# Optimization experiments

Hardware: AMD Instinct MI355X
Metric: run time of the kernel (lower is better)

## Reference

```python
import jax, jax.numpy as jnp
import numpy as np

B, T, D, H = 2, 2048, 1024, 16
DH = D // H
TOPK = 64


def setup_inputs() -> dict:
    key = jax.random.key(0)
    ks = jax.random.split(key, 10)
    s = D ** -0.5
    x = jax.random.normal(ks[0], (B, T, D), dtype=jnp.float32)
    key_padding_mask = jax.random.bernoulli(ks[1], 0.1, (B, T))
    Wq = jax.random.normal(ks[2], (D, D), dtype=jnp.float32) * s
    bq = jnp.zeros((D,), dtype=jnp.float32)
    Wk = jax.random.normal(ks[3], (D, D), dtype=jnp.float32) * s
    bk = jnp.zeros((D,), dtype=jnp.float32)
    Wv = jax.random.normal(ks[4], (D, D), dtype=jnp.float32) * s
    bv = jnp.zeros((D,), dtype=jnp.float32)
    Wo = jax.random.normal(ks[5], (D, D), dtype=jnp.float32) * s
    bo = jnp.zeros((D,), dtype=jnp.float32)
    return {"x": x, "Wq": Wq, "bq": bq, "Wk": Wk, "bk": bk,
            "Wv": Wv, "bv": bv, "Wo": Wo, "bo": bo,
            "key_padding_mask": key_padding_mask, "causal": 1}


def _attention(x, Wq, bq, Wk, bk, Wv, bv, Wo, bo, key_padding_mask, causal):
    b, t, d = x.shape
    dh = d // H

    def heads(y):  # (B,T,D) -> (B,H,T,Dh)
        return y.reshape(b, t, H, dh).transpose(0, 2, 1, 3)

    q = heads(x @ Wq.T + bq)
    k = heads(x @ Wk.T + bk)
    v = heads(x @ Wv.T + bv)

    scale = dh ** -0.5
    logits = jnp.einsum('bhqd,bhkd->bhqk', q, k) * scale  # (B,H,T,T)
    neg = jnp.finfo(logits.dtype).min

    # key padding mask: True blocks key position
    logits = jnp.where(key_padding_mask[:, None, None, :], neg, logits)

    if causal:
        i = jnp.arange(t)[:, None]
        j = jnp.arange(t)[None, :]
        blocked = j > (t - t + i)  # Tq == Tk
        logits = jnp.where(blocked[None, None], neg, logits)

    # hard top-k sparsification: keep top-k logits per row, rest -> -inf
    flat = logits.reshape(-1, t)  # (B*H*T, T)
    vals, idx = jax.lax.top_k(flat, TOPK)
    rows = jnp.arange(flat.shape[0])[:, None]
    sparse = jnp.full_like(flat, neg).at[rows, idx].set(vals)
    sparse = sparse.reshape(logits.shape)

    attn = jax.nn.softmax(sparse, axis=-1)
    out = jnp.einsum('bhqk,bhkd->bhqd', attn, v)  # (B,H,T,Dh)
    out = out.transpose(0, 2, 1, 3).reshape(b, t, d)
    return out @ Wo.T + bo


def reference(x, Wq, bq, Wk, bk, Wv, bv, Wo, bo, key_padding_mask, causal):
    return _attention(x, Wq, bq, Wk, bk, Wv, bv, Wo, bo, key_padding_mask, causal)
```

## Files before the change

kernel.cpp:

```cpp
#include <hip/hip_runtime.h>
#include <hip/hip_bf16.h>
#include <stdint.h>

#define BB 2
#define TT 2048
#define DD 1024
#define NH 16
#define HD 64
#define TOPK 64
#define NEGF (-3.402823466e38f)
#define ORD_NEG 0x00800000u
#define QT 16
#define KT 256
#define SELCAP 96

typedef short short8x __attribute__((ext_vector_type(8)));
typedef float floatx4 __attribute__((ext_vector_type(4)));

__device__ __forceinline__ uint32_t ord_u32(float x) {
    uint32_t b = __float_as_uint(x);
    return (b & 0x80000000u) ? ~b : (b | 0x80000000u);
}
__device__ __forceinline__ float unord(uint32_t u) {
    uint32_t b = (u & 0x80000000u) ? (u ^ 0x80000000u) : ~u;
    return __uint_as_float(b);
}
__device__ __forceinline__ short bf16_rne(float x) {
    uint32_t u = __float_as_uint(x);
    u += 0x7FFFu + ((u >> 16) & 1u);
    return (short)(u >> 16);
}
__device__ __forceinline__ float bf16_to_f(short h) {
    return __uint_as_float(((uint32_t)(uint16_t)h) << 16);
}
__device__ __forceinline__ bool mask_at(const void* m, int mode, int idx) {
    if (mode == 0) return ((const int*)m)[idx] != 0;
    if (mode == 1) return ((const unsigned char*)m)[idx] != 0;
    return ((const float*)m)[idx] != 0.0f;
}

__device__ __forceinline__ int dpp_wsum(int v) {
    v += __builtin_amdgcn_update_dpp(0, v, 0x111, 0xf, 0xf, true);
    v += __builtin_amdgcn_update_dpp(0, v, 0x112, 0xf, 0xf, true);
    v += __builtin_amdgcn_update_dpp(0, v, 0x114, 0xf, 0xf, true);
    v += __builtin_amdgcn_update_dpp(0, v, 0x118, 0xf, 0xf, true);
    v += __builtin_amdgcn_update_dpp(0, v, 0x142, 0xa, 0xf, true);
    v += __builtin_amdgcn_update_dpp(0, v, 0x143, 0xc, 0xf, true);
    return __builtin_amdgcn_readlane(v, 63);
}
__device__ __forceinline__ uint32_t dpp_wumax(uint32_t v) {
    uint32_t t;
    t = (uint32_t)__builtin_amdgcn_update_dpp(0, (int)v, 0x111, 0xf, 0xf, true); v = v > t ? v : t;
    t = (uint32_t)__builtin_amdgcn_update_dpp(0, (int)v, 0x112, 0xf, 0xf, true); v = v > t ? v : t;
    t = (uint32_t)__builtin_amdgcn_update_dpp(0, (int)v, 0x114, 0xf, 0xf, true); v = v > t ? v : t;
    t = (uint32_t)__builtin_amdgcn_update_dpp(0, (int)v, 0x118, 0xf, 0xf, true); v = v > t ? v : t;
    t = (uint32_t)__builtin_amdgcn_update_dpp(0, (int)v, 0x142, 0xa, 0xf, true); v = v > t ? v : t;
    t = (uint32_t)__builtin_amdgcn_update_dpp(0, (int)v, 0x143, 0xc, 0xf, true); v = v > t ? v : t;
    return (uint32_t)__builtin_amdgcn_readlane((int)v, 63);
}
__device__ __forceinline__ float dpp_fsum(float v) {
    v += __uint_as_float((uint32_t)__builtin_amdgcn_update_dpp(0, (int)__float_as_uint(v), 0x111, 0xf, 0xf, true));
    v += __uint_as_float((uint32_t)__builtin_amdgcn_update_dpp(0, (int)__float_as_uint(v), 0x112, 0xf, 0xf, true));
    v += __uint_as_float((uint32_t)__builtin_amdgcn_update_dpp(0, (int)__float_as_uint(v), 0x114, 0xf, 0xf, true));
    v += __uint_as_float((uint32_t)__builtin_amdgcn_update_dpp(0, (int)__float_as_uint(v), 0x118, 0xf, 0xf, true));
    v += __uint_as_float((uint32_t)__builtin_amdgcn_update_dpp(0, (int)__float_as_uint(v), 0x142, 0xa, 0xf, true));
    v += __uint_as_float((uint32_t)__builtin_amdgcn_update_dpp(0, (int)__float_as_uint(v), 0x143, 0xc, 0xf, true));
    return __uint_as_float((uint32_t)__builtin_amdgcn_readlane((int)__float_as_uint(v), 63));
}

__global__ void __launch_bounds__(1024) build_flags(
    const unsigned char* raw, const int* causalp, int* flags, uint32_t* Mt)
{
    __shared__ int odd_nz, big, s_mode;
    __shared__ uint32_t smt[BB * 64];
    const int tid = threadIdx.x;
    if (tid == 0) { odd_nz = 0; big = 0; }
    if (tid < BB * 64) smt[tid] = 0;
    __syncthreads();
    for (int i = tid; i < BB * TT; i += 1024) {
        unsigned char c = raw[i];
        if ((i & 3) && c) atomicOr(&odd_nz, 1);
        if (c > 1) atomicOr(&big, 1);
    }
    __syncthreads();
    if (tid == 0) {
        int mode = odd_nz ? (big ? 2 : 1) : 0;
        s_mode = mode;
        flags[0] = mode;
        flags[1] = (causalp[0] != 0) ? 1 : 0;
    }
    __syncthreads();
    const int mode = s_mode;
    const int w = tid >> 3, g = tid & 7;
    const int bb = w >> 6, l = w & 63;
    uint32_t bits = 0;
#pragma unroll
    for (int si = 0; si < 4; ++si) {
        int s = g * 4 + si;
        if (mask_at(raw, mode, bb * TT + l + 64 * s)) bits |= (1u << s);
    }
    if (bits) atomicOr(&smt[w], bits);
    __syncthreads();
    if (tid < BB * 64) Mt[tid] = smt[tid];
}

__global__ void __launch_bounds__(256) split_f32(
    const float* __restrict__ in, short* __restrict__ hi, short* __restrict__ lo,
    int n4, float scale)
{
    int i = blockIdx.x * blockDim.x + threadIdx.x;
    if (i >= n4) return;
    float4 v = ((const float4*)in)[i];
    float f[4] = {v.x * scale, v.y * scale, v.z * scale, v.w * scale};
    short hh[4], ll[4];
#pragma unroll
    for (int j = 0; j < 4; ++j) {
        hh[j] = bf16_rne(f[j]);
        ll[j] = bf16_rne(f[j] - bf16_to_f(hh[j]));
    }
    short4 h4; h4.x = hh[0]; h4.y = hh[1]; h4.z = hh[2]; h4.w = hh[3];
    short4 l4; l4.x = ll[0]; l4.y = ll[1]; l4.z = ll[2]; l4.w = ll[3];
    ((short4*)hi)[i] = h4;
    ((short4*)lo)[i] = l4;
}

__global__ void __launch_bounds__(256) split_w4(
    const float* __restrict__ W0, const float* __restrict__ W1,
    const float* __restrict__ W2, const float* __restrict__ W3,
    short* __restrict__ h0, short* __restrict__ l0, short* __restrict__ h1, short* __restrict__ l1,
    short* __restrict__ h2, short* __restrict__ l2, short* __restrict__ h3, short* __restrict__ l3,
    int n4)
{
    int i = blockIdx.x * blockDim.x + threadIdx.x;
    if (i >= n4) return;
    const int w = blockIdx.y;
    const float* in = (w == 0) ? W0 : (w == 1) ? W1 : (w == 2) ? W2 : W3;
    short* hi = (w == 0) ? h0 : (w == 1) ? h1 : (w == 2) ? h2 : h3;
    short* lo = (w == 0) ? l0 : (w == 1) ? l1 : (w == 2) ? l2 : l3;
    float4 v = ((const float4*)in)[i];
    float f[4] = {v.x, v.y, v.z, v.w};
    short hh[4], ll[4];
#pragma unroll
    for (int j = 0; j < 4; ++j) {
        hh[j] = bf16_rne(f[j]);
        ll[j] = bf16_rne(f[j] - bf16_to_f(hh[j]));
    }
    short4 h4; h4.x = hh[0]; h4.y = hh[1]; h4.z = hh[2]; h4.w = hh[3];
    short4 l4; l4.x = ll[0]; l4.y = ll[1]; l4.z = ll[2]; l4.w = ll[3];
    ((short4*)hi)[i] = h4;
    ((short4*)lo)[i] = l4;
}

__global__ void __launch_bounds__(256) gemm_bf16s(
    const short* __restrict__ Ah, const short* __restrict__ Al,
    const short* __restrict__ Bh, const short* __restrict__ Bl,
    const float* __restrict__ bias, float* __restrict__ Cf,
    short* __restrict__ Ch, short* __restrict__ Cl, float scale, int mode)
{
    const int tid = threadIdx.x, lane = tid & 63, wv = tid >> 6;
    const int wr = wv >> 1, wc = wv & 1;
    const int m0 = blockIdx.y * 128 + wr * 64;
    const int n0 = blockIdx.x * 64 + wc * 32;
    const int lrow = lane & 15, lk = (lane >> 4) * 8;

    floatx4 acc[4][2];
#pragma unroll
    for (int i = 0; i < 4; ++i)
#pragma unroll
        for (int j = 0; j < 2; ++j) acc[i][j] = (floatx4){0.f, 0.f, 0.f, 0.f};

    auto ldfr = [&](int kk, short8x* pah, short8x* pal, short8x* pbh, short8x* pbl) {
#pragma unroll
        for (int mb = 0; mb < 4; ++mb) {
            size_t off = (size_t)(m0 + mb * 16 + lrow) * DD + kk + lk;
            pah[mb] = *(const short8x*)(Ah + off);
            pal[mb] = *(const short8x*)(Al + off);
        }
#pragma unroll
        for (int nb = 0; nb < 2; ++nb) {
            size_t off = (size_t)(n0 + nb * 16 + lrow) * DD + kk + lk;
            pbh[nb] = *(const short8x*)(Bh + off);
            pbl[nb] = *(const short8x*)(Bl + off);
        }
    };
    auto domfma = [&](short8x* pah, short8x* pal, short8x* pbh, short8x* pbl) {
#pragma unroll
        for (int mb = 0; mb < 4; ++mb)
#pragma unroll
            for (int nb = 0; nb < 2; ++nb) {
                acc[mb][nb] = __builtin_amdgcn_mfma_f32_16x16x32_bf16(pah[mb], pbh[nb], acc[mb][nb], 0, 0, 0);
                acc[mb][nb] = __builtin_amdgcn_mfma_f32_16x16x32_bf16(pah[mb], pbl[nb], acc[mb][nb], 0, 0, 0);
                acc[mb][nb] = __builtin_amdgcn_mfma_f32_16x16x32_bf16(pal[mb], pbh[nb], acc[mb][nb], 0, 0, 0);
            }
    };

    short8x A0[4], L0[4], B0[2], C0[2];
    short8x A1[4], L1[4], B1[2], C1[2];
    ldfr(0, A0, L0, B0, C0);
    for (int kk = 0; kk < DD; kk += 64) {
        ldfr(kk + 32, A1, L1, B1, C1);
        domfma(A0, L0, B0, C0);
        if (kk + 64 < DD) ldfr(kk + 64, A0, L0, B0, C0);
        domfma(A1, L1, B1, C1);
    }

#pragma unroll
    for (int mb = 0; mb < 4; ++mb)
#pragma unroll
        for (int nb = 0; nb < 2; ++nb) {
            int n = n0 + nb * 16 + lrow;
            float bv = bias[n];
#pragma unroll
            for (int j = 0; j < 4; ++j) {
                int m = m0 + mb * 16 + (lane >> 4) * 4 + j;
                float v = acc[mb][nb][j] + bv;
                if (mode == 0) {
                    Cf[(size_t)m * DD + n] = v;
                } else {
                    int b = m >> 11, t = m & (TT - 1), h = n >> 6, dh = n & (HD - 1);
                    size_t idx = (((size_t)b * NH + h) * TT + t) * HD + dh;
                    if (mode == 1) {
                        Cf[idx] = v;
                    } else {
                        v *= scale;
                        short hi16 = bf16_rne(v);
                        Ch[idx] = hi16;
                        Cl[idx] = bf16_rne(v - bf16_to_f(hi16));
                    }
                }
            }
        }
}

__global__ void __launch_bounds__(256) gemm_xwt(
    const float* __restrict__ A, const float* __restrict__ W,
    const float* __restrict__ bias, float* __restrict__ C,
    int M, int N, int K, int split_heads)
{
    __shared__ float As[64][17];
    __shared__ float Ws[64][17];
    const int tid = threadIdx.x;
    const int tx = tid & 15, ty = tid >> 4;
    const int arow = blockIdx.y * 64, bcol = blockIdx.x * 64;
    float acc[4][4] = {};

    for (int k0 = 0; k0 < K; k0 += 16) {
        const int r = tid >> 2, c = (tid & 3) * 4;
        float4 a4 = *(const float4*)(A + (size_t)(arow + r) * K + k0 + c);
        As[r][c] = a4.x; As[r][c + 1] = a4.y; As[r][c + 2] = a4.z; As[r][c + 3] = a4.w;
        float4 w4 = *(const float4*)(W + (size_t)(bcol + r) * K + k0 + c);
        Ws[r][c] = w4.x; Ws[r][c + 1] = w4.y; Ws[r][c + 2] = w4.z; Ws[r][c + 3] = w4.w;
        __syncthreads();
#pragma unroll
        for (int k = 0; k < 16; ++k) {
            float a0 = As[ty * 4 + 0][k], a1 = As[ty * 4 + 1][k];
            float a2 = As[ty * 4 + 2][k], a3 = As[ty * 4 + 3][k];
            float w0 = Ws[tx * 4 + 0][k], w1 = Ws[tx * 4 + 1][k];
            float w2 = Ws[tx * 4 + 2][k], w3 = Ws[tx * 4 + 3][k];
            acc[0][0] += a0 * w0; acc[0][1] += a0 * w1; acc[0][2] += a0 * w2; acc[0][3] += a0 * w3;
            acc[1][0] += a1 * w0; acc[1][1] += a1 * w1; acc[1][2] += a1 * w2; acc[1][3] += a1 * w3;
            acc[2][0] += a2 * w0; acc[2][1] += a2 * w1; acc[2][2] += a2 * w2; acc[2][3] += a2 * w3;
            acc[3][0] += a3 * w0; acc[3][1] += a3 * w1; acc[3][2] += a3 * w2; acc[3][3] += a3 * w3;
        }
        __syncthreads();
    }

#pragma unroll
    for (int i = 0; i < 4; ++i) {
        int m = arow + ty * 4 + i;
#pragma unroll
        for (int j = 0; j < 4; ++j) {
            int n = bcol + tx * 4 + j;
            float v = acc[i][j] + bias[n];
            if (split_heads) {
                int b = m / TT, t = m % TT, h = n / HD, dh = n % HD;
                C[(((size_t)b * NH + h) * TT + t) * HD + dh] = v;
            } else {
                C[(size_t)m * N + n] = v;
            }
        }
    }
}

__global__ void __launch_bounds__(1024) attn_topk(
    const short* __restrict__ Qhi, const short* __restrict__ Qlo,
    const short* __restrict__ Khi, const short* __restrict__ Klo,
    const float* __restrict__ V, const uint32_t* __restrict__ Mt,
    const int* __restrict__ flags, float* __restrict__ O)
{
    __shared__ float s_S[2][QT][KT + 1];
    __shared__ int2  s_sel[QT][SELCAP];

    const int tid = threadIdx.x, lane = tid & 63, wv = tid >> 6;
    const int qt = blockIdx.x, bh = blockIdx.y;
    const int b = bh >> 4, h = bh & 15;
    const int causal = flags[1];
    const size_t hb = (size_t)bh * (size_t)TT * HD;
    const int r0 = qt * QT;
    const int gq = r0 + wv;
    const float* __restrict__ Vh = V + hb;

    short8x qhi[2], qlo[2];
    {
        const size_t qoff = hb + (size_t)(r0 + (lane & 15)) * HD + (lane >> 4) * 8;
        qhi[0] = *(const short8x*)(Qhi + qoff);
        qhi[1] = *(const short8x*)(Qhi + qoff + 32);
        qlo[0] = *(const short8x*)(Qlo + qoff);
        qlo[1] = *(const short8x*)(Qlo + qoff + 32);
    }

    const uint32_t mwords = Mt[b * 64 + lane];

    uint32_t lgo[32];
#pragma unroll
    for (int i = 0; i < 32; ++i) lgo[i] = ORD_NEG;

    const int lastT = causal ? ((r0 + QT - 1) >> 8) : 7;

#pragma unroll
    for (int t = 0; t < 8; ++t) {
        if (t <= lastT) {
            const size_t koff = hb + (size_t)(t * KT + wv * 16 + (lane & 15)) * HD + (lane >> 4) * 8;
            short8x kh0 = *(const short8x*)(Khi + koff);
            short8x kh1 = *(const short8x*)(Khi + koff + 32);
            short8x kl0 = *(const short8x*)(Klo + koff);
            short8x kl1 = *(const short8x*)(Klo + koff + 32);
            floatx4 acc = {0.f, 0.f, 0.f, 0.f};
            acc = __builtin_amdgcn_mfma_f32_16x16x32_bf16(qhi[0], kh0, acc, 0, 0, 0);
            acc = __builtin_amdgcn_mfma_f32_16x16x32_bf16(qhi[0], kl0, acc, 0, 0, 0);
            acc = __builtin_amdgcn_mfma_f32_16x16x32_bf16(qlo[0], kh0, acc, 0, 0, 0);
            acc = __builtin_amdgcn_mfma_f32_16x16x32_bf16(qhi[1], kh1, acc, 0, 0, 0);
            acc = __builtin_amdgcn_mfma_f32_16x16x32_bf16(qhi[1], kl1, acc, 0, 0, 0);
            acc = __builtin_amdgcn_mfma_f32_16x16x32_bf16(qlo[1], kh1, acc, 0, 0, 0);
#pragma unroll
            for (int j = 0; j < 4; ++j)
                s_S[t & 1][(lane >> 4) * 4 + j][wv * 16 + (lane & 15)] = acc[j];
            __syncthreads();
#pragma unroll
            for (int j = 0; j < 4; ++j) {
                float sv = s_S[t & 1][wv][j * 64 + lane];
                int key = t * KT + j * 64 + lane;
                bool blocked = ((mwords >> (t * 4 + j)) & 1u) || (causal && key > gq);
                lgo[t * 4 + j] = blocked ? ORD_NEG : ord_u32(sv);
            }
        }
    }

    uint32_t moL = 0; int nvL = 0;
#pragma unroll
    for (int i = 0; i < 32; ++i) {
        uint32_t u = lgo[i];
        moL = u > moL ? u : moL;
        nvL += (u > ORD_NEG) ? 1 : 0;
    }
    const uint32_t mo = dpp_wumax(moL);
    const int nv = dpp_wsum(nvL);

    auto wcount = [&](uint32_t thrv) -> int {
        int c = 0;
#pragma unroll
        for (int i = 0; i < 32; ++i) c += (lgo[i] >= thrv) ? 1 : 0;
        return dpp_wsum(c);
    };

    float outv;
    if (nv == 0) {
        float a0 = 0.f, a1 = 0.f, a2 = 0.f, a3 = 0.f;
        for (int j = 0; j < TT; j += 4) {
            a0 += Vh[(j + 0) * HD + lane];
            a1 += Vh[(j + 1) * HD + lane];
            a2 += Vh[(j + 2) * HD + lane];
            a3 += Vh[(j + 3) * HD + lane];
        }
        outv = (a0 + a1 + a2 + a3) * (1.0f / TT);
    } else {
        const float mF = unord(mo);
        uint32_t thr = 0; uint32_t lo_b = 0, hi_b = 0; int done = 0;
        {
            uint32_t p1 = ord_u32(mF - 2.0f);
            int c1 = wcount(p1);
            if (c1 == TOPK) { thr = p1; done = 1; }
            else if (c1 > TOPK) { lo_b = p1; hi_b = mo; }
            else {
                uint32_t p2 = ord_u32(mF - 4.0f);
                int c2 = wcount(p2);
                if (c2 == TOPK) { thr = p2; done = 1; }
                else if (c2 > TOPK) { lo_b = p2; hi_b = p1; }
                else {
                    uint32_t p3 = ord_u32(mF - 15.0f);
                    int c3 = wcount(p3);
                    if (c3 <= TOPK) { thr = p3; done = 1; }
                    else { lo_b = p3; hi_b = p2; }
                }
            }
        }
        if (!done) {
            while (hi_b - lo_b > 1u) {
                uint32_t mid = lo_b + ((hi_b - lo_b) >> 1);
                int c = wcount(mid);
                if (c == TOPK) { lo_b = mid; break; }
                if (c > TOPK) lo_b = mid; else hi_b = mid;
            }
            thr = lo_b;
        }

        int nsel = 0; float Sp = 0.f;
#pragma unroll
        for (int i = 0; i < 32; ++i) {
            uint32_t u = lgo[i];
            float w = 0.f;
            if (u >= thr) w = __expf(unord(u) - mF);
            Sp += w;
            nsel += (w > 0.f) ? 1 : 0;
            lgo[i] = (w > 0.f) ? __float_as_uint(w) : 0u;
        }
        const float S = dpp_fsum(Sp);
        int incl = nsel;
#pragma unroll
        for (int off = 1; off < 64; off <<= 1) {
            int t2 = __shfl_up(incl, off, 64);
            if (lane >= off) incl += t2;
        }
        int base = incl - nsel;
        int cnt  = __builtin_amdgcn_readlane(incl, 63);
        int pos = base;
#pragma unroll
        for (int i = 0; i < 32; ++i) {
            uint32_t wbits = lgo[i];
            if (wbits) {
                if (pos < SELCAP) {
                    int keyoff = (((i >> 2) * KT + (i & 3) * 64 + lane) << 6);
                    s_sel[wv][pos] = make_int2(keyoff, (int)wbits);
                }
                ++pos;
            }
        }
        if (cnt > SELCAP) cnt = SELCAP;
        float acc = 0.f;
        int i2 = 0;
        for (; i2 + 4 <= cnt; i2 += 4) {
            int2 e0 = s_sel[wv][i2],     e1 = s_sel[wv][i2 + 1];
            int2 e2 = s_sel[wv][i2 + 2], e3 = s_sel[wv][i2 + 3];
            acc += __int_as_float(e0.y) * Vh[e0.x + lane];
            acc += __int_as_float(e1.y) * Vh[e1.x + lane];
            acc += __int_as_float(e2.y) * Vh[e2.x + lane];
            acc += __int_as_float(e3.y) * Vh[e3.x + lane];
        }
        for (; i2 < cnt; ++i2) {
            int2 e = s_sel[wv][i2];
            acc += __int_as_float(e.y) * Vh[e.x + lane];
        }
        outv = acc / S;
    }
    O[((size_t)b * TT + gq) * DD + h * HD + lane] = outv;
}

extern "C" void kernel_launch(void* const* d_in, const int* in_sizes, int n_in,
                              void* d_out, int out_size, void* d_ws, size_t ws_size,
                              hipStream_t stream) {
    const float* x  = (const float*)d_in[0];
    const float* Wq = (const float*)d_in[1];
    const float* bq = (const float*)d_in[2];
    const float* Wk = (const float*)d_in[3];
    const float* bk = (const float*)d_in[4];
    const float* Wv = (const float*)d_in[5];
    const float* bv = (const float*)d_in[6];
    const float* Wo = (const float*)d_in[7];
    const float* bo = (const float*)d_in[8];
    const void*  maskp = d_in[9];
    const int*   causalp = (const int*)d_in[10];
    float* out = (float*)d_out;

    char* ws = (char*)d_ws;
    const size_t TEN  = (size_t)BB * TT * DD * sizeof(float);
    const size_t HTEN = TEN / 2;
    const size_t WSZ  = (size_t)DD * DD * 2;
    const size_t NEED = 6 * TEN + 4096;

    const int nx4 = BB * TT * DD / 4, nw4 = DD * DD / 4;
    dim3 gg(DD / 64, (BB * TT) / 128);
    dim3 ag(TT / QT, BB * NH);

    if (ws_size >= NEED) {
        float* O    = (float*)(ws);
        float* Vf   = (float*)(ws + TEN);
        short* xh   = (short*)(ws + 2 * TEN);
        short* xl   = (short*)(ws + 2 * TEN + HTEN);
        short* Qhi  = (short*)(ws + 3 * TEN);
        short* Qlo  = (short*)(ws + 3 * TEN + HTEN);
        short* Khi  = (short*)(ws + 4 * TEN);
        short* Klo  = (short*)(ws + 4 * TEN + HTEN);
        char*  wb   = ws + 5 * TEN;
        short* wqh = (short*)(wb);            short* wql = (short*)(wb + WSZ);
        short* wkh = (short*)(wb + 2 * WSZ);  short* wkl = (short*)(wb + 3 * WSZ);
        short* wvh = (short*)(wb + 4 * WSZ);  short* wvl = (short*)(wb + 5 * WSZ);
        short* woh = (short*)(wb + 6 * WSZ);  short* wol = (short*)(wb + 7 * WSZ);
        int*      flags = (int*)(wb + 8 * WSZ);
        uint32_t* Mt    = (uint32_t*)(wb + 8 * WSZ + 256);

        build_flags<<<1, 1024, 0, stream>>>((const unsigned char*)maskp, causalp, flags, Mt);

        split_f32<<<(nx4 + 255) / 256, 256, 0, stream>>>(x, xh, xl, nx4, 1.0f);
        dim3 wg((nw4 + 255) / 256, 4);
        split_w4<<<wg, 256, 0, stream>>>(Wq, Wk, Wv, Wo,
                                         wqh, wql, wkh, wkl, wvh, wvl, woh, wol, nw4);

        gemm_bf16s<<<gg, 256, 0, stream>>>(xh, xl, wqh, wql, bq, nullptr, Qhi, Qlo, 0.125f, 2);
        gemm_bf16s<<<gg, 256, 0, stream>>>(xh, xl, wkh, wkl, bk, nullptr, Khi, Klo, 1.0f, 2);
        gemm_bf16s<<<gg, 256, 0, stream>>>(xh, xl, wvh, wvl, bv, Vf, nullptr, nullptr, 1.0f, 1);

        attn_topk<<<ag, 1024, 0, stream>>>(Qhi, Qlo, Khi, Klo, Vf, Mt, flags, O);

        split_f32<<<(nx4 + 255) / 256, 256, 0, stream>>>(O, xh, xl, nx4, 1.0f);
        gemm_bf16s<<<gg, 256, 0, stream>>>(xh, xl, woh, wol, bo, out, nullptr, nullptr, 1.0f, 0);
    } else {
        float* Qf  = (float*)(ws);
        float* Kf  = (float*)(ws + TEN);
        float* Vf  = (float*)(ws + 2 * TEN);
        float* O   = (float*)(ws + 3 * TEN);
        short* Qhi = (short*)(ws + 4 * TEN);
        short* Qlo = (short*)(ws + 4 * TEN + HTEN);
        short* Khi = (short*)(ws + 5 * TEN);
        short* Klo = (short*)(ws + 5 * TEN + HTEN);
        int*      flags = (int*)(ws + 6 * TEN);
        uint32_t* Mt    = (uint32_t*)(ws + 6 * TEN + 256);

        build_flags<<<1, 1024, 0, stream>>>((const unsigned char*)maskp, causalp, flags, Mt);
        dim3 g2(DD / 64, (BB * TT) / 64);
        gemm_xwt<<<g2, 256, 0, stream>>>(x, Wq, bq, Qf, BB * TT, DD, DD, 1);
        gemm_xwt<<<g2, 256, 0, stream>>>(x, Wk, bk, Kf, BB * TT, DD, DD, 1);
        gemm_xwt<<<g2, 256, 0, stream>>>(x, Wv, bv, Vf, BB * TT, DD, DD, 1);
        split_f32<<<(nx4 + 255) / 256, 256, 0, stream>>>(Qf, Qhi, Qlo, nx4, 0.125f);
        split_f32<<<(nx4 + 255) / 256, 256, 0, stream>>>(Kf, Khi, Klo, nx4, 1.0f);
        attn_topk<<<ag, 1024, 0, stream>>>(Qhi, Qlo, Khi, Klo, Vf, Mt, flags, O);
        gemm_xwt<<<g2, 256, 0, stream>>>(O, Wo, bo, out, BB * TT, DD, DD, 0);
    }
}
```

Measured before the change: 817.4 us.

## Fuse O bf16 split into attention, shrink GEMM tiles, XCD-aware grid, ballot compaction

The attention kernel now writes its output directly as bf16 hi/lo pairs, which removes the separate split_f32 pass and the fp32 O buffer before the output projection. The GEMM tile drops from 128x64 to 64x64 per block, giving more blocks and fewer registers per thread. The attention grid is flattened and remapped so consecutive blocks on the same XCD share a head, aiming for better L2 reuse of K and V. Selection compaction uses ballot/mbcnt instead of a shuffle prefix scan, and V gathers use scalar readfirstlane offsets. Smaller GEMM tiles lower the operand reuse per load.

Result: slower. 876.7 us (+7.3%).

```diff
diff --git a/kernel.cpp b/kernel.cpp
--- a/kernel.cpp
+++ b/kernel.cpp
@@ -158,20 +158,19 @@
     short* __restrict__ Ch, short* __restrict__ Cl, float scale, int mode)
 {
     const int tid = threadIdx.x, lane = tid & 63, wv = tid >> 6;
-    const int wr = wv >> 1, wc = wv & 1;
-    const int m0 = blockIdx.y * 128 + wr * 64;
-    const int n0 = blockIdx.x * 64 + wc * 32;
+    const int m0 = blockIdx.y * 64 + (wv >> 1) * 32;
+    const int n0 = blockIdx.x * 64 + (wv & 1) * 32;
     const int lrow = lane & 15, lk = (lane >> 4) * 8;
 
-    floatx4 acc[4][2];
-#pragma unroll
-    for (int i = 0; i < 4; ++i)
+    floatx4 acc[2][2];
+#pragma unroll
+    for (int i = 0; i < 2; ++i)
 #pragma unroll
         for (int j = 0; j < 2; ++j) acc[i][j] = (floatx4){0.f, 0.f, 0.f, 0.f};
 
     auto ldfr = [&](int kk, short8x* pah, short8x* pal, short8x* pbh, short8x* pbl) {
 #pragma unroll
-        for (int mb = 0; mb < 4; ++mb) {
+        for (int mb = 0; mb < 2; ++mb) {
             size_t off = (size_t)(m0 + mb * 16 + lrow) * DD + kk + lk;
             pah[mb] = *(const short8x*)(Ah + off);
             pal[mb] = *(const short8x*)(Al + off);
@@ -185,7 +184,7 @@
     };
     auto domfma = [&](short8x* pah, short8x* pal, short8x* pbh, short8x* pbl) {
 #pragma unroll
-        for (int mb = 0; mb < 4; ++mb)
+        for (int mb = 0; mb < 2; ++mb)
 #pragma unroll
             for (int nb = 0; nb < 2; ++nb) {
                 acc[mb][nb] = __builtin_amdgcn_mfma_f32_16x16x32_bf16(pah[mb], pbh[nb], acc[mb][nb], 0, 0, 0);
@@ -194,8 +193,8 @@
             }
     };
 
-    short8x A0[4], L0[4], B0[2], C0[2];
-    short8x A1[4], L1[4], B1[2], C1[2];
+    short8x A0[2], L0[2], B0[2], C0[2];
+    short8x A1[2], L1[2], B1[2], C1[2];
     ldfr(0, A0, L0, B0, C0);
     for (int kk = 0; kk < DD; kk += 64) {
         ldfr(kk + 32, A1, L1, B1, C1);
@@ -205,7 +204,7 @@
     }
 
 #pragma unroll
-    for (int mb = 0; mb < 4; ++mb)
+    for (int mb = 0; mb < 2; ++mb)
 #pragma unroll
         for (int nb = 0; nb < 2; ++nb) {
             int n = n0 + nb * 16 + lrow;
@@ -286,19 +285,24 @@
     const short* __restrict__ Qhi, const short* __restrict__ Qlo,
     const short* __restrict__ Khi, const short* __restrict__ Klo,
     const float* __restrict__ V, const uint32_t* __restrict__ Mt,
-    const int* __restrict__ flags, float* __restrict__ O)
+    const int* __restrict__ flags, short* __restrict__ Ohi,
+    short* __restrict__ Olo, float* __restrict__ Of)
 {
     __shared__ float s_S[2][QT][KT + 1];
     __shared__ int2  s_sel[QT][SELCAP];
 
     const int tid = threadIdx.x, lane = tid & 63, wv = tid >> 6;
-    const int qt = blockIdx.x, bh = blockIdx.y;
+    const int d = blockIdx.x;
+    const int xcd = d & 7, chunk = d >> 3;
+    const int bh = (xcd << 2) | (chunk >> 7);
+    const int qt = chunk & 127;
     const int b = bh >> 4, h = bh & 15;
     const int causal = flags[1];
     const size_t hb = (size_t)bh * (size_t)TT * HD;
     const int r0 = qt * QT;
     const int gq = r0 + wv;
     const float* __restrict__ Vh = V + hb;
+    const float* __restrict__ Vl = Vh + lane;
 
     short8x qhi[2], qlo[2];
     {
@@ -404,55 +408,70 @@
             thr = lo_b;
         }
 
-        int nsel = 0; float Sp = 0.f;
+        int dummy = 0; (void)dummy;
+        float Sp = 0.f;
 #pragma unroll
         for (int i = 0; i < 32; ++i) {
             uint32_t u = lgo[i];
             float w = 0.f;
             if (u >= thr) w = __expf(unord(u) - mF);
             Sp += w;
-            nsel += (w > 0.f) ? 1 : 0;
             lgo[i] = (w > 0.f) ? __float_as_uint(w) : 0u;
         }
         const float S = dpp_fsum(Sp);
-        int incl = nsel;
-#pragma unroll
-        for (int off = 1; off < 64; off <<= 1) {
-            int t2 = __shfl_up(incl, off, 64);
-            if (lane >= off) incl += t2;
-        }
-        int base = incl - nsel;
-        int cnt  = __builtin_amdgcn_readlane(incl, 63);
-        int pos = base;
+
+        int base = 0;
 #pragma unroll
         for (int i = 0; i < 32; ++i) {
             uint32_t wbits = lgo[i];
+            unsigned long long msk = __ballot(wbits != 0);
             if (wbits) {
+                int below = __builtin_amdgcn_mbcnt_hi((uint32_t)(msk >> 32),
+                            __builtin_amdgcn_mbcnt_lo((uint32_t)msk, 0));
+                int pos = base + below;
                 if (pos < SELCAP) {
                     int keyoff = (((i >> 2) * KT + (i & 3) * 64 + lane) << 6);
                     s_sel[wv][pos] = make_int2(keyoff, (int)wbits);
                 }
-                ++pos;
-            }
-        }
-        if (cnt > SELCAP) cnt = SELCAP;
+            }
+            base += (int)__popcll(msk);
+        }
+        int cnt = base < SELCAP ? base : SELCAP;
+
         float acc = 0.f;
         int i2 = 0;
         for (; i2 + 4 <= cnt; i2 += 4) {
             int2 e0 = s_sel[wv][i2],     e1 = s_sel[wv][i2 + 1];
             int2 e2 = s_sel[wv][i2 + 2], e3 = s_sel[wv][i2 + 3];
-            acc += __int_as_float(e0.y) * Vh[e0.x + lane];
-            acc += __int_as_float(e1.y) * Vh[e1.x + lane];
-            acc += __int_as_float(e2.y) * Vh[e2.x + lane];
-            acc += __int_as_float(e3.y) * Vh[e3.x + lane];
+            int k0 = __builtin_amdgcn_readfirstlane(e0.x);
+            int k1 = __builtin_amdgcn_readfirstlane(e1.x);
+            int k2 = __builtin_amdgcn_readfirstlane(e2.x);
+            int k3 = __builtin_amdgcn_readfirstlane(e3.x);
+            float w0 = __uint_as_float((uint32_t)__builtin_amdgcn_readfirstlane(e0.y));
+            float w1 = __uint_as_float((uint32_t)__builtin_amdgcn_readfirstlane(e1.y));
+            float w2 = __uint_as_float((uint32_t)__builtin_amdgcn_readfirstlane(e2.y));
+            float w3 = __uint_as_float((uint32_t)__builtin_amdgcn_readfirstlane(e3.y));
+            acc += w0 * Vl[k0];
+            acc += w1 * Vl[k1];
+            acc += w2 * Vl[k2];
+            acc += w3 * Vl[k3];
         }
         for (; i2 < cnt; ++i2) {
             int2 e = s_sel[wv][i2];
-            acc += __int_as_float(e.y) * Vh[e.x + lane];
+            int k = __builtin_amdgcn_readfirstlane(e.x);
+            float w = __uint_as_float((uint32_t)__builtin_amdgcn_readfirstlane(e.y));
+            acc += w * Vl[k];
         }
         outv = acc / S;
     }
-    O[((size_t)b * TT + gq) * DD + h * HD + lane] = outv;
+    const size_t oidx = ((size_t)b * TT + gq) * DD + h * HD + lane;
+    if (Of) {
+        Of[oidx] = outv;
+    } else {
+        short hi16 = bf16_rne(outv);
+        Ohi[oidx] = hi16;
+        Olo[oidx] = bf16_rne(outv - bf16_to_f(hi16));
+    }
 }
 
 extern "C" void kernel_launch(void* const* d_in, const int* in_sizes, int n_in,
@@ -478,18 +497,18 @@
     const size_t NEED = 6 * TEN + 4096;
 
     const int nx4 = BB * TT * DD / 4, nw4 = DD * DD / 4;
-    dim3 gg(DD / 64, (BB * TT) / 128);
-    dim3 ag(TT / QT, BB * NH);
+    dim3 gg(DD / 64, (BB * TT) / 64);
 
     if (ws_size >= NEED) {
-        float* O    = (float*)(ws);
-        float* Vf   = (float*)(ws + TEN);
-        short* xh   = (short*)(ws + 2 * TEN);
-        short* xl   = (short*)(ws + 2 * TEN + HTEN);
-        short* Qhi  = (short*)(ws + 3 * TEN);
-        short* Qlo  = (short*)(ws + 3 * TEN + HTEN);
-        short* Khi  = (short*)(ws + 4 * TEN);
-        short* Klo  = (short*)(ws + 4 * TEN + HTEN);
+        float* Vf   = (float*)(ws);
+        short* xh   = (short*)(ws + TEN);
+        short* xl   = (short*)(ws + TEN + HTEN);
+        short* Qhi  = (short*)(ws + 2 * TEN);
+        short* Qlo  = (short*)(ws + 2 * TEN + HTEN);
+        short* Khi  = (short*)(ws + 3 * TEN);
+        short* Klo  = (short*)(ws + 3 * TEN + HTEN);
+        short* Ohi  = (short*)(ws + 4 * TEN);
+        short* Olo  = (short*)(ws + 4 * TEN + HTEN);
         char*  wb   = ws + 5 * TEN;
         short* wqh = (short*)(wb);            short* wql = (short*)(wb + WSZ);
         short* wkh = (short*)(wb + 2 * WSZ);  short* wkl = (short*)(wb + 3 * WSZ);
@@ -509,10 +528,10 @@
         gemm_bf16s<<<gg, 256, 0, stream>>>(xh, xl, wkh, wkl, bk, nullptr, Khi, Klo, 1.0f, 2);
         gemm_bf16s<<<gg, 256, 0, stream>>>(xh, xl, wvh, wvl, bv, Vf, nullptr, nullptr, 1.0f, 1);
 
-        attn_topk<<<ag, 1024, 0, stream>>>(Qhi, Qlo, Khi, Klo, Vf, Mt, flags, O);
-
-        split_f32<<<(nx4 + 255) / 256, 256, 0, stream>>>(O, xh, xl, nx4, 1.0f);
-        gemm_bf16s<<<gg, 256, 0, stream>>>(xh, xl, woh, wol, bo, out, nullptr, nullptr, 1.0f, 0);
+        attn_topk<<<BB * NH * (TT / QT), 1024, 0, stream>>>(Qhi, Qlo, Khi, Klo, Vf, Mt, flags,
+                                                            Ohi, Olo, nullptr);
+
+        gemm_bf16s<<<gg, 256, 0, stream>>>(Ohi, Olo, woh, wol, bo, out, nullptr, nullptr, 1.0f, 0);
     } else {
         float* Qf  = (float*)(ws);
         float* Kf  = (float*)(ws + TEN);
@@ -532,7 +551,8 @@
         gemm_xwt<<<g2, 256, 0, stream>>>(x, Wv, bv, Vf, BB * TT, DD, DD, 1);
         split_f32<<<(nx4 + 255) / 256, 256, 0, stream>>>(Qf, Qhi, Qlo, nx4, 0.125f);
         split_f32<<<(nx4 + 255) / 256, 256, 0, stream>>>(Kf, Khi, Klo, nx4, 1.0f);
-        attn_topk<<<ag, 1024, 0, stream>>>(Qhi, Qlo, Khi, Klo, Vf, Mt, flags, O);
+        attn_topk<<<BB * NH * (TT / QT), 1024, 0, stream>>>(Qhi, Qlo, Khi, Klo, Vf, Mt, flags,
+                                                            nullptr, nullptr, O);
         gemm_xwt<<<g2, 256, 0, stream>>>(O, Wo, bo, out, BB * TT, DD, DD, 0);
     }
 }
```
